# Performance work log

Measured on AMD Instinct MI355X. Metric: run time of the kernel, lower is better.

Reference implementation:

```python
import jax, jax.numpy as jnp
import numpy as np

DIM = 1024
HEADS = 16
HEAD_DIM = DIM // HEADS


def setup_inputs() -> dict:
    key = jax.random.key(0)
    ks = jax.random.split(key, 10)
    B, N, M = 4, 2048, 2048
    s = 1.0 / np.sqrt(DIM)
    return {
        "x": jax.random.normal(ks[0], (B, N, DIM), jnp.float32),
        "context": jax.random.normal(ks[1], (B, M, DIM), jnp.float32),
        "Wq": jax.random.normal(ks[2], (DIM, DIM), jnp.float32) * s,
        "bq": jnp.zeros((DIM,), jnp.float32),
        "Wk": jax.random.normal(ks[3], (DIM, DIM), jnp.float32) * s,
        "bk": jnp.zeros((DIM,), jnp.float32),
        "Wv": jax.random.normal(ks[4], (DIM, DIM), jnp.float32) * s,
        "bv": jnp.zeros((DIM,), jnp.float32),
        "Wo": jax.random.normal(ks[5], (DIM, DIM), jnp.float32) * s,
        "bo": jnp.zeros((DIM,), jnp.float32),
    }


def reference(x, context, Wq, bq, Wk, bk, Wv, bv, Wo, bo):
    B, N, C = x.shape
    M = context.shape[1]
    scale = HEAD_DIM ** (-0.5)
    # projections + split heads: [B, H, L, D]
    q = (x @ Wq.T + bq).reshape(B, N, HEADS, HEAD_DIM).transpose(0, 2, 1, 3)
    k = (context @ Wk.T + bk).reshape(B, M, HEADS, HEAD_DIM).transpose(0, 2, 1, 3)
    v = (context @ Wv.T + bv).reshape(B, M, HEADS, HEAD_DIM).transpose(0, 2, 1, 3)
    attn = jax.nn.softmax(jnp.einsum('bhnd,bhmd->bhnm', q, k) * scale, axis=-1)
    out = jnp.einsum('bhnm,bhmd->bhnd', attn, v)  # [B, H, N, D]
    out = out.transpose(0, 2, 1, 3).reshape(B, N, C)
    return out @ Wo.T + bo
```

## Files before the change

### kernel.cpp

```cpp
#include <hip/hip_runtime.h>
#include <hip/hip_bf16.h>
#include <stdint.h>


#define HEADS 16
#define HD 64
#define NSEQ 2048
#define DIMSZ 1024

typedef __bf16 bf16x8_t __attribute__((ext_vector_type(8)));
typedef float f32x4_t __attribute__((ext_vector_type(4)));
typedef short s16x4 __attribute__((ext_vector_type(4)));
typedef unsigned short u16;
typedef unsigned int u32;

__device__ __forceinline__ u16 f2bf(float f) {
    union { float f; u32 i; } x; x.f = f;
    u32 r = x.i + 0x7FFF + ((x.i >> 16) & 1);
    return (u16)(r >> 16);
}
__device__ __forceinline__ u32 pk2(float a, float b) {
    __hip_bfloat162 h = __float22bfloat162_rn(float2{a, b});
    union { __hip_bfloat162 h2; u32 u; } c; c.h2 = h; return c.u;
}

#if defined(__has_builtin)
#if __has_builtin(__builtin_amdgcn_exp2f)
#define EXP2(x) __builtin_amdgcn_exp2f(x)
#endif
#endif
#ifndef EXP2
#define EXP2(x) exp2f(x)
#endif

__device__ __forceinline__ void pl32swap(u32& a, u32& b) {
    asm("v_permlane32_swap_b32 %0, %1" : "+v"(a), "+v"(b));
}
__device__ __forceinline__ void pl16swap(u32& a, u32& b) {
    asm("v_permlane16_swap_b32 %0, %1" : "+v"(a), "+v"(b));
}

#define GLDS(g, l) __builtin_amdgcn_global_load_lds( \
    (const __attribute__((address_space(1))) void*)(g), \
    (__attribute__((address_space(3))) void*)(l), 16, 0, 0)

__global__ __launch_bounds__(256)
void cvt_all(const float* __restrict__ x, const float* __restrict__ ctx,
             const float* __restrict__ wq, const float* __restrict__ wk,
             const float* __restrict__ wv, const float* __restrict__ wo,
             u16* __restrict__ xb, u16* __restrict__ ctxb,
             u16* __restrict__ wqb, u16* __restrict__ wkb,
             u16* __restrict__ wvb, u16* __restrict__ wob)
{
    long g = (long)blockIdx.x * 256 + threadIdx.x;
    const float* in; u16* out; long off;
    if (g < 1048576L)      { in = x;   out = xb;   off = g; }
    else if (g < 2097152L) { in = ctx; out = ctxb; off = g - 1048576L; }
    else if (g < 2228224L) { in = wq;  out = wqb;  off = g - 2097152L; }
    else if (g < 2359296L) { in = wk;  out = wkb;  off = g - 2228224L; }
    else if (g < 2490368L) { in = wv;  out = wvb;  off = g - 2359296L; }
    else                   { in = wo;  out = wob;  off = g - 2490368L; }
    long i = off * 8;
    float4 a = *(const float4*)(in + i);
    float4 b = *(const float4*)(in + i + 4);
    union { uint4 v; u16 h[8]; } u;
    u.h[0] = f2bf(a.x); u.h[1] = f2bf(a.y); u.h[2] = f2bf(a.z); u.h[3] = f2bf(a.w);
    u.h[4] = f2bf(b.x); u.h[5] = f2bf(b.y); u.h[6] = f2bf(b.z); u.h[7] = f2bf(b.w);
    *(uint4*)(out + i) = u.v;
}

#define BM 128
#define BN 128

#define BKQ 64

__global__ __launch_bounds__(256, 3)
void qkv_gemm(const u16* __restrict__ xb, const u16* __restrict__ ctxb,
              const u16* __restrict__ wq, const u16* __restrict__ wk,
              const u16* __restrict__ wv,
              const float* __restrict__ bq, const float* __restrict__ bk,
              const float* __restrict__ bv,
              u16* __restrict__ qo, u16* __restrict__ ko, u16* __restrict__ vo,
              float qscale)
{
    __shared__ __align__(16) u16 Asm[BM * BKQ];
    __shared__ __align__(16) u16 Wsm[BN * BKQ];

    const int lin  = blockIdx.x + 24 * blockIdx.y;
    const int lin2 = (lin & 7) * 192 + (lin >> 3);
    const int bx   = lin2 % 24;
    const int by   = lin2 / 24;

    const int g    = bx >> 3;
    const int col0 = (bx & 7) * BN;
    const int row0 = by * BM;

    const u16* A = (g == 0) ? xb : ctxb;
    const u16* W = (g == 0) ? wq : (g == 1) ? wk : wv;
    const float* bias = (g == 0) ? bq : (g == 1) ? bk : bv;
    const float scale = (g == 0) ? qscale : 1.0f;

    const int t    = threadIdx.x;
    const int lane = t & 63;
    const int wid  = t >> 6;
    const int lrow = lane & 15;
    const int lq   = lane >> 4;
    const int wm   = (wid >> 1) * 64;
    const int wn   = (wid & 1) * 64;

    const u16* gA[4]; const u16* gW[4];
    u16* lA[4]; u16* lW[4];
    #pragma unroll
    for (int q = 0; q < 4; q++) {
        int s = q * 256 + t;
        int r = s >> 3;
        int c = (s & 7) ^ (r & 7);
        gA[q] = A + (long)(row0 + r) * DIMSZ + c * 8;
        gW[q] = W + (long)(col0 + r) * DIMSZ + c * 8;
        int lofs = (q * 256 + wid * 64) * 8;
        lA[q] = &Asm[lofs];
        lW[q] = &Wsm[lofs];
    }

    f32x4_t zero = {0.f, 0.f, 0.f, 0.f};
    f32x4_t acc[4][4];
    #pragma unroll
    for (int i = 0; i < 4; i++)
        #pragma unroll
        for (int j = 0; j < 4; j++) acc[i][j] = zero;

    const int rsw = lrow & 7;

    if (g < 2) {
        for (int k0 = 0; k0 < DIMSZ; k0 += BKQ) {
            __syncthreads();
            #pragma unroll
            for (int q = 0; q < 4; q++) {
                GLDS(gA[q] + k0, lA[q]);
                GLDS(gW[q] + k0, lW[q]);
            }
            __syncthreads();

            #pragma unroll
            for (int kk = 0; kk < 2; kk++) {
                bf16x8_t af[4], bfr[4];
                #pragma unroll
                for (int i = 0; i < 4; i++)
                    af[i] = *(const bf16x8_t*)
                        &Asm[(wm + 16 * i + lrow) * BKQ + (((kk * 4 + lq) ^ rsw) << 3)];
                #pragma unroll
                for (int j = 0; j < 4; j++)
                    bfr[j] = *(const bf16x8_t*)
                        &Wsm[(wn + 16 * j + lrow) * BKQ + (((kk * 4 + lq) ^ rsw) << 3)];
                #pragma unroll
                for (int i = 0; i < 4; i++)
                    #pragma unroll
                    for (int j = 0; j < 4; j++)
                        acc[i][j] = __builtin_amdgcn_mfma_f32_16x16x32_bf16(
                            bfr[j], af[i], acc[i][j], 0, 0, 0);
            }
        }

        u16* outp = g ? ko : qo;
        #pragma unroll
        for (int j = 0; j < 4; j++) {
            int d0 = col0 + wn + 16 * j + lq * 4;
            f32x4_t bb = *(const f32x4_t*)&bias[d0];
            int h  = d0 >> 6;
            int dl = d0 & 63;
            #pragma unroll
            for (int i = 0; i < 4; i++) {
                int n  = row0 + wm + 16 * i + lrow;
                int b  = n >> 11, nn = n & 2047;
                uint2 p;
                p.x = pk2((acc[i][j][0] + bb[0]) * scale,
                          (acc[i][j][1] + bb[1]) * scale);
                p.y = pk2((acc[i][j][2] + bb[2]) * scale,
                          (acc[i][j][3] + bb[3]) * scale);
                long oidx = ((long)((b * HEADS + h) * NSEQ + nn) << 6) + dl;
                *(uint2*)&outp[oidx] = p;
            }
        }
    } else {
        for (int k0 = 0; k0 < DIMSZ; k0 += BKQ) {
            __syncthreads();
            #pragma unroll
            for (int q = 0; q < 4; q++) {
                GLDS(gA[q] + k0, lA[q]);
                GLDS(gW[q] + k0, lW[q]);
            }
            __syncthreads();

            #pragma unroll
            for (int kk = 0; kk < 2; kk++) {
                bf16x8_t af[4], bfr[4];
                #pragma unroll
                for (int i = 0; i < 4; i++)
                    af[i] = *(const bf16x8_t*)
                        &Asm[(wm + 16 * i + lrow) * BKQ + (((kk * 4 + lq) ^ rsw) << 3)];
                #pragma unroll
                for (int j = 0; j < 4; j++)
                    bfr[j] = *(const bf16x8_t*)
                        &Wsm[(wn + 16 * j + lrow) * BKQ + (((kk * 4 + lq) ^ rsw) << 3)];
                #pragma unroll
                for (int i = 0; i < 4; i++)
                    #pragma unroll
                    for (int j = 0; j < 4; j++)
                        acc[i][j] = __builtin_amdgcn_mfma_f32_16x16x32_bf16(
                            af[i], bfr[j], acc[i][j], 0, 0, 0);
            }
        }

        float bvv[4];
        #pragma unroll
        for (int j = 0; j < 4; j++) bvv[j] = bias[col0 + wn + 16 * j + lrow];

        #pragma unroll
        for (int i = 0; i < 4; i++) {
            int n0 = row0 + wm + 16 * i + lq * 4;
            int b  = n0 >> 11, nn = n0 & 2047;
            #pragma unroll
            for (int j = 0; j < 4; j++) {
                int d = col0 + wn + 16 * j + lrow;
                uint2 p;
                p.x = pk2(acc[i][j][0] + bvv[j], acc[i][j][1] + bvv[j]);
                p.y = pk2(acc[i][j][2] + bvv[j], acc[i][j][3] + bvv[j]);
                long o = ((long)((b * HEADS + (d >> 6)) * HD + (d & 63)) << 11) + nn;
                *(uint2*)&vo[o] = p;
            }
        }
    }
}

#define BKO 64

__global__ __launch_bounds__(256, 2)
void gemm_o(const u16* __restrict__ A, const u16* __restrict__ W,
            const float* __restrict__ bias, float* __restrict__ out)
{
    __shared__ __align__(16) u16 Asm[2][BM * BKO];
    __shared__ __align__(16) u16 Wsm[2][BN * BKO];

    const int lin  = blockIdx.x + 8 * blockIdx.y;
    const int lin2 = (lin & 7) * 64 + (lin >> 3);
    const int col0 = (lin2 & 7) * BN;
    const int row0 = (lin2 >> 3) * BM;

    const int t    = threadIdx.x;
    const int lane = t & 63;
    const int wid  = t >> 6;
    const int lrow = lane & 15;
    const int lq   = lane >> 4;
    const int wm   = (wid >> 1) * 64;
    const int wn   = (wid & 1) * 64;

    const u16* gA[4]; const u16* gW[4]; int lofs[4];
    #pragma unroll
    for (int q = 0; q < 4; q++) {
        int s = q * 256 + t;
        int r = s >> 3;
        int c = (s & 7) ^ (r & 7);
        gA[q] = A + (long)(row0 + r) * DIMSZ + c * 8;
        gW[q] = W + (long)(col0 + r) * DIMSZ + c * 8;
        lofs[q] = (q * 256 + wid * 64) * 8;
    }

    f32x4_t zero = {0.f, 0.f, 0.f, 0.f};
    f32x4_t acc[4][4];
    #pragma unroll
    for (int i = 0; i < 4; i++)
        #pragma unroll
        for (int j = 0; j < 4; j++) acc[i][j] = zero;

    const int rsw = lrow & 7;

    auto stage = [&](int k0, int nb) {
        #pragma unroll
        for (int q = 0; q < 4; q++) {
            GLDS(gA[q] + k0, &Asm[nb][lofs[q]]);
            GLDS(gW[q] + k0, &Wsm[nb][lofs[q]]);
        }
    };
    auto compute = [&](int nb) {
        #pragma unroll
        for (int kk = 0; kk < 2; kk++) {
            bf16x8_t af[4], bfr[4];
            #pragma unroll
            for (int i = 0; i < 4; i++)
                af[i] = *(const bf16x8_t*)
                    &Asm[nb][(wm + 16 * i + lrow) * BKO + (((kk * 4 + lq) ^ rsw) << 3)];
            #pragma unroll
            for (int j = 0; j < 4; j++)
                bfr[j] = *(const bf16x8_t*)
                    &Wsm[nb][(wn + 16 * j + lrow) * BKO + (((kk * 4 + lq) ^ rsw) << 3)];
            #pragma unroll
            for (int i = 0; i < 4; i++)
                #pragma unroll
                for (int j = 0; j < 4; j++)
                    acc[i][j] = __builtin_amdgcn_mfma_f32_16x16x32_bf16(
                        bfr[j], af[i], acc[i][j], 0, 0, 0);
        }
    };

    stage(0, 0);
    __syncthreads();

    for (int k0 = 0; k0 < DIMSZ; k0 += 2 * BKO) {
        stage(k0 + BKO, 1);
        compute(0);
        __syncthreads();
        if (k0 + 2 * BKO < DIMSZ) stage(k0 + 2 * BKO, 0);
        compute(1);
        __syncthreads();
    }

    #pragma unroll
    for (int j = 0; j < 4; j++) {
        int d0 = col0 + wn + 16 * j + lq * 4;
        f32x4_t bb = *(const f32x4_t*)&bias[d0];
        #pragma unroll
        for (int i = 0; i < 4; i++) {
            int n = row0 + wm + 16 * i + lrow;
            f32x4_t v;
            #pragma unroll
            for (int r = 0; r < 4; r++) v[r] = acc[i][j][r] + bb[r];
            *(f32x4_t*)&out[(long)n * DIMSZ + d0] = v;
        }
    }
}

__global__ __launch_bounds__(512, 4)
void attn(const u16* __restrict__ Q, const u16* __restrict__ K,
          const u16* __restrict__ Vt, u16* __restrict__ O)
{
    __shared__ __align__(16) u16 Ksm[2][64 * 64];
    __shared__ __align__(16) u16 Vsm[2][64 * 64];

    const int t    = threadIdx.x;
    const int lane = t & 63;
    const int w    = t >> 6;
    const int lrow = lane & 15;
    const int lq   = lane >> 4;
    const int bh   = blockIdx.x;
    const int q0   = blockIdx.y * 256;
    const int b    = bh >> 4;
    const int h    = bh & 15;

    bf16x8_t qf[2][2];
    #pragma unroll
    for (int qa = 0; qa < 2; qa++) {
        const long qbase = ((long)bh * NSEQ + q0 + w * 32 + qa * 16 + lrow) * HD;
        qf[qa][0] = *(const bf16x8_t*)&Q[qbase + lq * 8];
        qf[qa][1] = *(const bf16x8_t*)&Q[qbase + lq * 8 + 32];
    }

    const long kvbase = (long)bh * NSEQ * HD;

    const int sr = t >> 3;
    const int sc = (t & 7) ^ (sr & 7);
    const u16* gK0 = K  + kvbase + (long)sr * HD + sc * 8;
    const u16* gV0 = Vt + kvbase + (long)sr * NSEQ + sc * 8;
    const int lofs = (w * 64) * 8;

    f32x4_t zero = {0.f, 0.f, 0.f, 0.f};
    f32x4_t oacc[2][4];
    #pragma unroll
    for (int qa = 0; qa < 2; qa++)
        #pragma unroll
        for (int jd = 0; jd < 4; jd++) oacc[qa][jd] = zero;
    f32x4_t lacc[2] = {zero, zero};

    union { u32 u[4]; bf16x8_t v; } ob;
    ob.u[0] = ob.u[1] = ob.u[2] = ob.u[3] = 0x3F803F80u;
    const bf16x8_t onesb = ob.v;

    const int rsw = lrow & 7;

    auto stage = [&](int ktn, int nb) {
        GLDS(gK0 + (long)ktn * (64 * HD), &Ksm[nb][lofs]);
        GLDS(gV0 + ktn * 64,              &Vsm[nb][lofs]);
    };

    auto tile = [&](const u16* Ks, const u16* Vs) {
        #pragma unroll
        for (int t2 = 0; t2 < 2; t2++) {
            f32x4_t sacc[2][2];
            __builtin_amdgcn_s_setprio(1);
            #pragma unroll
            for (int jh = 0; jh < 2; jh++) {
                int jt = t2 * 2 + jh;
                bf16x8_t kf0 = *(const bf16x8_t*)
                    &Ks[(16 * jt + lrow) * 64 + ((lq ^ rsw) << 3)];
                bf16x8_t kf1 = *(const bf16x8_t*)
                    &Ks[(16 * jt + lrow) * 64 + (((4 + lq) ^ rsw) << 3)];
                sacc[jh][0] = __builtin_amdgcn_mfma_f32_16x16x32_bf16(
                    kf0, qf[0][0], zero, 0, 0, 0);
                sacc[jh][1] = __builtin_amdgcn_mfma_f32_16x16x32_bf16(
                    kf0, qf[1][0], zero, 0, 0, 0);
                sacc[jh][0] = __builtin_amdgcn_mfma_f32_16x16x32_bf16(
                    kf1, qf[0][1], sacc[jh][0], 0, 0, 0);
                sacc[jh][1] = __builtin_amdgcn_mfma_f32_16x16x32_bf16(
                    kf1, qf[1][1], sacc[jh][1], 0, 0, 0);
            }
            __builtin_amdgcn_s_setprio(0);

            bf16x8_t pa32[2];
            #pragma unroll
            for (int qa = 0; qa < 2; qa++) {
                u32 uu[2][2];
                #pragma unroll
                for (int jh = 0; jh < 2; jh++) {
                    float p0 = EXP2(sacc[jh][qa][0]);
                    float p1 = EXP2(sacc[jh][qa][1]);
                    float p2 = EXP2(sacc[jh][qa][2]);
                    float p3 = EXP2(sacc[jh][qa][3]);
                    uu[jh][0] = pk2(p0, p1);
                    uu[jh][1] = pk2(p2, p3);
                }
                pl32swap(uu[0][0], uu[1][0]);
                pl16swap(uu[0][0], uu[1][0]);
                pl32swap(uu[0][1], uu[1][1]);
                pl16swap(uu[0][1], uu[1][1]);
                union { u32 u[4]; bf16x8_t v; } pk_;
                pk_.u[0] = uu[0][0]; pk_.u[1] = uu[0][1];
                pk_.u[2] = uu[1][0]; pk_.u[3] = uu[1][1];
                pa32[qa] = pk_.v;
            }

            __builtin_amdgcn_s_setprio(1);
            lacc[0] = __builtin_amdgcn_mfma_f32_16x16x32_bf16(
                pa32[0], onesb, lacc[0], 0, 0, 0);
            lacc[1] = __builtin_amdgcn_mfma_f32_16x16x32_bf16(
                pa32[1], onesb, lacc[1], 0, 0, 0);
            #pragma unroll
            for (int jd = 0; jd < 4; jd++) {
                bf16x8_t vb = *(const bf16x8_t*)
                    &Vs[(16 * jd + lrow) * 64 + (((4 * t2 + lq) ^ rsw) << 3)];
                oacc[0][jd] = __builtin_amdgcn_mfma_f32_16x16x32_bf16(
                    pa32[0], vb, oacc[0][jd], 0, 0, 0);
                oacc[1][jd] = __builtin_amdgcn_mfma_f32_16x16x32_bf16(
                    pa32[1], vb, oacc[1][jd], 0, 0, 0);
            }
            __builtin_amdgcn_s_setprio(0);
        }
    };

    stage(0, 0);
    __syncthreads();

    for (int kt = 0; kt < NSEQ / 64; kt += 2) {
        stage(kt + 1, 1);
        tile(Ksm[0], Vsm[0]);
        __syncthreads();
        if (kt + 2 < NSEQ / 64) stage(kt + 2, 0);
        tile(Ksm[1], Vsm[1]);
        __syncthreads();
    }

    float linv[2][4];
    #pragma unroll
    for (int qa = 0; qa < 2; qa++)
        #pragma unroll
        for (int r = 0; r < 4; r++)
            linv[qa][r] = __builtin_amdgcn_rcpf(lacc[qa][r]);

    #pragma unroll
    for (int qa = 0; qa < 2; qa++) {
        #pragma unroll
        for (int jd = 0; jd < 4; jd++) {
            #pragma unroll
            for (int r = 0; r < 4; r++) {
                int qrow = q0 + w * 32 + qa * 16 + lq * 4 + r;
                int d    = 16 * jd + lrow;
                long oidx = ((long)(b * NSEQ + qrow)) * DIMSZ + h * HD + d;
                O[oidx] = f2bf(oacc[qa][jd][r] * linv[qa][r]);
            }
        }
    }
}

extern "C" void kernel_launch(void* const* d_in, const int* in_sizes, int n_in,
                              void* d_out, int out_size, void* d_ws, size_t ws_size,
                              hipStream_t stream)
{
    const float* x   = (const float*)d_in[0];
    const float* ctx = (const float*)d_in[1];
    const float* Wq  = (const float*)d_in[2];
    const float* bq  = (const float*)d_in[3];
    const float* Wk  = (const float*)d_in[4];
    const float* bk  = (const float*)d_in[5];
    const float* Wv  = (const float*)d_in[6];
    const float* bv  = (const float*)d_in[7];
    const float* Wo  = (const float*)d_in[8];
    const float* bo  = (const float*)d_in[9];
    float* out = (float*)d_out;

    const size_t NX = (size_t)8192 * 1024;
    const size_t NW = (size_t)1024 * 1024;

    u16* xb   = (u16*)d_ws;
    u16* ctxb = xb + NX;
    u16* wqb  = ctxb + NX;
    u16* wkb  = wqb + NW;
    u16* wvb  = wkb + NW;
    u16* wob  = wvb + NW;
    u16* qws  = wob + NW;
    u16* kws  = qws + NX;
    u16* vws  = kws + NX;
    u16* aws  = xb;

    cvt_all<<<10240, 256, 0, stream>>>(x, ctx, Wq, Wk, Wv, Wo,
                                       xb, ctxb, wqb, wkb, wvb, wob);

    const float qscale = 0.125f * 1.44269504088896340736f;

    qkv_gemm<<<dim3(24, 8192 / BM), 256, 0, stream>>>(
        xb, ctxb, wqb, wkb, wvb, bq, bk, bv, qws, kws, vws, qscale);
    attn<<<dim3(64, NSEQ / 256), 512, 0, stream>>>(qws, kws, vws, aws);
    gemm_o<<<dim3(DIMSZ / BN, 8192 / BM), 256, 0, stream>>>(aws, wob, bo, out);
}
```

Baseline: 296.8 us.

## Drop double buffering in output GEMM and raise occupancy bounds

The output projection GEMM goes from a double-buffered LDS pipeline to a single buffer. Each K step now loads, syncs, then computes, which halves LDS use per block. Both GEMMs get launch bounds allowing 4 blocks per CU instead of 3 or 2. The aim is to hide latency through more resident blocks rather than in-block prefetch, at the cost of an extra barrier per step, no overlap of loads with MFMA inside a block, and tighter register limits that could cause spills.

```diff
diff --git a/kernel.cpp b/kernel.cpp
--- a/kernel.cpp
+++ b/kernel.cpp
@@ -74,7 +74,7 @@
 
 #define BKQ 64
 
-__global__ __launch_bounds__(256, 3)
+__global__ __launch_bounds__(256, 4)
 void qkv_gemm(const u16* __restrict__ xb, const u16* __restrict__ ctxb,
               const u16* __restrict__ wq, const u16* __restrict__ wk,
               const u16* __restrict__ wv,
@@ -234,12 +234,12 @@
 
 #define BKO 64
 
-__global__ __launch_bounds__(256, 2)
+__global__ __launch_bounds__(256, 4)
 void gemm_o(const u16* __restrict__ A, const u16* __restrict__ W,
             const float* __restrict__ bias, float* __restrict__ out)
 {
-    __shared__ __align__(16) u16 Asm[2][BM * BKO];
-    __shared__ __align__(16) u16 Wsm[2][BN * BKO];
+    __shared__ __align__(16) u16 Asm[BM * BKO];
+    __shared__ __align__(16) u16 Wsm[BN * BKO];
 
     const int lin  = blockIdx.x + 8 * blockIdx.y;
     const int lin2 = (lin & 7) * 64 + (lin >> 3);
@@ -254,7 +254,8 @@
     const int wm   = (wid >> 1) * 64;
     const int wn   = (wid & 1) * 64;
 
-    const u16* gA[4]; const u16* gW[4]; int lofs[4];
+    const u16* gA[4]; const u16* gW[4];
+    u16* lA[4]; u16* lW[4];
     #pragma unroll
     for (int q = 0; q < 4; q++) {
         int s = q * 256 + t;
@@ -262,7 +263,9 @@
         int c = (s & 7) ^ (r & 7);
         gA[q] = A + (long)(row0 + r) * DIMSZ + c * 8;
         gW[q] = W + (long)(col0 + r) * DIMSZ + c * 8;
-        lofs[q] = (q * 256 + wid * 64) * 8;
+        int lofs = (q * 256 + wid * 64) * 8;
+        lA[q] = &Asm[lofs];
+        lW[q] = &Wsm[lofs];
     }
 
     f32x4_t zero = {0.f, 0.f, 0.f, 0.f};
@@ -274,25 +277,26 @@
 
     const int rsw = lrow & 7;
 
-    auto stage = [&](int k0, int nb) {
+    for (int k0 = 0; k0 < DIMSZ; k0 += BKO) {
+        __syncthreads();
         #pragma unroll
         for (int q = 0; q < 4; q++) {
-            GLDS(gA[q] + k0, &Asm[nb][lofs[q]]);
-            GLDS(gW[q] + k0, &Wsm[nb][lofs[q]]);
-        }
-    };
-    auto compute = [&](int nb) {
+            GLDS(gA[q] + k0, lA[q]);
+            GLDS(gW[q] + k0, lW[q]);
+        }
+        __syncthreads();
+
         #pragma unroll
         for (int kk = 0; kk < 2; kk++) {
             bf16x8_t af[4], bfr[4];
             #pragma unroll
             for (int i = 0; i < 4; i++)
                 af[i] = *(const bf16x8_t*)
-                    &Asm[nb][(wm + 16 * i + lrow) * BKO + (((kk * 4 + lq) ^ rsw) << 3)];
+                    &Asm[(wm + 16 * i + lrow) * BKO + (((kk * 4 + lq) ^ rsw) << 3)];
             #pragma unroll
             for (int j = 0; j < 4; j++)
                 bfr[j] = *(const bf16x8_t*)
-                    &Wsm[nb][(wn + 16 * j + lrow) * BKO + (((kk * 4 + lq) ^ rsw) << 3)];
+                    &Wsm[(wn + 16 * j + lrow) * BKO + (((kk * 4 + lq) ^ rsw) << 3)];
             #pragma unroll
             for (int i = 0; i < 4; i++)
                 #pragma unroll
@@ -300,18 +304,6 @@
                     acc[i][j] = __builtin_amdgcn_mfma_f32_16x16x32_bf16(
                         bfr[j], af[i], acc[i][j], 0, 0, 0);
         }
-    };
-
-    stage(0, 0);
-    __syncthreads();
-
-    for (int k0 = 0; k0 < DIMSZ; k0 += 2 * BKO) {
-        stage(k0 + BKO, 1);
-        compute(0);
-        __syncthreads();
-        if (k0 + 2 * BKO < DIMSZ) stage(k0 + 2 * BKO, 0);
-        compute(1);
-        __syncthreads();
     }
 
     #pragma unroll
```

After: 344.0 us. +15.9%, slower.
